# Kernel tuning notes

Hardware: AMD Instinct MI355X
Metric: run time of the kernel (lower is better)

The kernel has to match this reference:

```python
import jax, jax.numpy as jnp
import numpy as np

B, HW, ENC = 64, 14, 2048
T_CAP, VOCAB = 25, 10000
EMB = DEC = ATT = 512


def setup_inputs() -> dict:
    key = jax.random.key(0)
    ks = jax.random.split(key, 24)
    n = lambda k, shape, s=0.02: jax.random.normal(k, shape, jnp.float32) * s
    encoder_out = jax.random.normal(ks[0], (B, HW, HW, ENC), jnp.float32)
    captions = jax.random.randint(ks[1], (B, T_CAP), 0, VOCAB)
    lens = jax.random.randint(ks[2], (B,), 2, T_CAP + 1)
    caption_lengths = jnp.sort(lens)[::-1].at[0].set(T_CAP)  # sorted desc, max=T_CAP
    return {
        'encoder_out': encoder_out,
        'captions': captions,
        'caption_lengths': caption_lengths,
        'emb': jax.random.uniform(ks[3], (VOCAB, EMB), jnp.float32, -0.1, 0.1),
        'We_att': n(ks[4], (ENC, ATT)), 'be_att': jnp.zeros((ATT,), jnp.float32),
        'Wd_att': n(ks[5], (DEC, ATT)), 'bd_att': jnp.zeros((ATT,), jnp.float32),
        'v_att': n(ks[6], (ATT, 1)),    'bv_att': jnp.zeros((1,), jnp.float32),
        'W_ih': n(ks[7], (4 * DEC, EMB + ENC)), 'b_ih': jnp.zeros((4 * DEC,), jnp.float32),
        'W_hh': n(ks[8], (4 * DEC, DEC)),       'b_hh': jnp.zeros((4 * DEC,), jnp.float32),
        'W_init_h': n(ks[9], (ENC, DEC)),  'b_init_h': jnp.zeros((DEC,), jnp.float32),
        'W_init_c': n(ks[10], (ENC, DEC)), 'b_init_c': jnp.zeros((DEC,), jnp.float32),
        'W_fbeta': n(ks[11], (DEC, ENC)),  'b_fbeta': jnp.zeros((ENC,), jnp.float32),
        'W_fc': jax.random.uniform(ks[12], (DEC, VOCAB), jnp.float32, -0.1, 0.1),
        'b_fc': jnp.zeros((VOCAB,), jnp.float32),
    }


def reference(encoder_out, captions, caption_lengths, emb,
              We_att, be_att, Wd_att, bd_att, v_att, bv_att,
              W_ih, b_ih, W_hh, b_hh,
              W_init_h, b_init_h, W_init_c, b_init_c,
              W_fbeta, b_fbeta, W_fc, b_fc):
    Bn = encoder_out.shape[0]
    enc = encoder_out.reshape(Bn, -1, encoder_out.shape[-1])  # [B, P=196, ENC]
    decode_lengths = caption_lengths - 1
    T = captions.shape[1] - 1  # static max(decode_lengths)

    emb_cap = emb[captions]                    # [B, T+1, EMB]
    mean_enc = enc.mean(axis=1)                # [B, ENC]
    h0 = mean_enc @ W_init_h + b_init_h        # [B, DEC]
    c0 = mean_enc @ W_init_c + b_init_c
    att1 = enc @ We_att + be_att               # [B, P, ATT], hoisted (same math each step)

    def step(carry, inp):
        h, c = carry
        x_emb, active = inp                    # [B,EMB], [B] bool (batch_size_t mask)
        # attention
        att2 = h @ Wd_att + bd_att             # [B, ATT]
        e = (jax.nn.relu(att1 + att2[:, None, :]) @ v_att)[..., 0] + bv_att[0]  # [B, P]
        alpha = jax.nn.softmax(e, axis=1)
        ctx = jnp.einsum('bp,bpe->be', alpha, enc)
        # gated context
        ctx = jax.nn.sigmoid(h @ W_fbeta + b_fbeta) * ctx
        # LSTMCell (torch gate order i, f, g, o)
        x = jnp.concatenate([x_emb, ctx], axis=1)
        g = x @ W_ih.T + b_ih + h @ W_hh.T + b_hh
        i_g, f_g, g_g, o_g = jnp.split(g, 4, axis=1)
        c_new = jax.nn.sigmoid(f_g) * c + jax.nn.sigmoid(i_g) * jnp.tanh(g_g)
        h_new = jax.nn.sigmoid(o_g) * jnp.tanh(c_new)
        pred = h_new @ W_fc + b_fc             # dropout = identity (eval)
        m = active[:, None]
        pred = jnp.where(m, pred, 0.0)         # padded rows stay zero (as in torch)
        alpha = jnp.where(m, alpha, 0.0)
        h = jnp.where(m, h_new, h)
        c = jnp.where(m, c_new, c)
        return (h, c), (pred, alpha)

    active_ts = jnp.arange(T)[:, None] < decode_lengths[None, :]   # [T, B]
    xs = (jnp.swapaxes(emb_cap[:, :T], 0, 1), active_ts)
    _, (preds, alphas) = jax.lax.scan(step, (h0, c0), xs)
    predictions = jnp.swapaxes(preds, 0, 1)    # [B, T, VOCAB]
    alphas = jnp.swapaxes(alphas, 0, 1)        # [B, T, P]
    return predictions, captions, decode_lengths, alphas
```

## Files before the change

### kernel.cpp

```cpp
#include <hip/hip_runtime.h>
#include <hip/hip_bf16.h>

#define BATCH 64
#define NPIX 196
#define ENCD 2048
#define ATTD 512
#define DECD 512
#define EMBD 512
#define NVOCAB 10000
#define TSTEPS 24
#define KX 3072
#define NPAD 10112

typedef short bf16x8 __attribute__((ext_vector_type(8)));
typedef float f32x4 __attribute__((ext_vector_type(4)));

__device__ inline ushort f2bf(float f) {
    union { float f; unsigned u; } v; v.f = f;
    unsigned r = (v.u + 0x7fff + ((v.u >> 16) & 1)) >> 16;
    return (ushort)r;
}
__device__ inline float bf2f(ushort u) {
    union { unsigned u; float f; } v; v.u = ((unsigned)u) << 16;
    return v.f;
}

__global__ __launch_bounds__(256) void k_prep(
        const float* __restrict__ Wih, const float* __restrict__ Whh,
        const float* __restrict__ Wd, const float* __restrict__ Wfb,
        const float* __restrict__ Wfc, const float* __restrict__ We,
        const float* __restrict__ emb, const int* __restrict__ caps,
        const int* __restrict__ lens,
        ushort* __restrict__ WTj, ushort* __restrict__ BpreT,
        ushort* __restrict__ WfcT, ushort* __restrict__ WeT,
        ushort* __restrict__ embpartb, float* __restrict__ hcacc,
        float* __restrict__ cap_out, float* __restrict__ len_out) {
    __shared__ float tile[32][33];
    int blk = blockIdx.x, tid = threadIdx.x;
    if (blk < 2048) {
        int j = blk;
        for (int k = tid; k < KX; k += 256) {
            float v = (k < 2560) ? Wih[(size_t)j * 2560 + k] : Whh[(size_t)j * 512 + (k - 2560)];
            WTj[(size_t)j * KX + k] = f2bf(v);
        }
        if (blk == 0) {
            for (int i = tid; i < 1664; i += 256) {
                if (i < 1600) cap_out[i] = (float)caps[i];
                else          len_out[i - 1600] = (float)(lens[i - 1600] - 1);
            }
        }
    } else if (blk < 3328) {
        int i = blk - 2048;
        int nb = (i % 80) * 32, kb = (i / 80) * 32;
        int tx = tid & 31, ty = tid >> 5;
        for (int s = 0; s < 32; s += 8) {
            int k = kb + ty + s, n = nb + tx;
            float v = (n < ATTD) ? Wd[(size_t)k * ATTD + n] : Wfb[(size_t)k * ENCD + (n - ATTD)];
            tile[ty + s][tx] = v;
        }
        __syncthreads();
        for (int s = 0; s < 32; s += 8)
            BpreT[(size_t)(nb + ty + s) * 512 + kb + tx] = f2bf(tile[tx][ty + s]);
    } else if (blk < 8384) {
        int i = blk - 3328;
        int nb = (i % 316) * 32, kb = (i / 316) * 32;
        int tx = tid & 31, ty = tid >> 5;
        for (int s = 0; s < 32; s += 8) {
            int k = kb + ty + s, n = nb + tx;
            float v = (n < NVOCAB) ? Wfc[(size_t)k * NVOCAB + n] : 0.f;
            tile[ty + s][tx] = v;
        }
        __syncthreads();
        for (int s = 0; s < 32; s += 8)
            WfcT[(size_t)(nb + ty + s) * 512 + kb + tx] = f2bf(tile[tx][ty + s]);
    } else if (blk < 9408) {
        int i = blk - 8384;
        int nb = (i % 16) * 32, kb = (i / 16) * 32;
        int tx = tid & 31, ty = tid >> 5;
        for (int s = 0; s < 32; s += 8) {
            int k = kb + ty + s, n = nb + tx;
            tile[ty + s][tx] = We[(size_t)k * ATTD + n];
        }
        __syncthreads();
        for (int s = 0; s < 32; s += 8)
            WeT[(size_t)(nb + ty + s) * ENCD + kb + tx] = f2bf(tile[tx][ty + s]);
    } else if (blk < 10176) {
        int i = blk - 9408;
        int r0 = (i % 24) * 64;
        int n0 = (i / 24) * 64;
        int w = tid >> 6, l = tid & 63;
        int m = l & 15, kg = l >> 4;
        int n = n0 + w * 16 + m;
        const float* Bp = Wih + (size_t)n * 2560 + kg * 8;
        int tok[4];
#pragma unroll
        for (int mf = 0; mf < 4; ++mf) {
            int row = r0 + m + mf * 16;
            tok[mf] = caps[(row & 63) * 25 + (row >> 6)];
        }
        f32x4 acc[4] = {};
        for (int k0 = 0; k0 < 512; k0 += 32) {
            float4 b0 = *(const float4*)(Bp + k0);
            float4 b1 = *(const float4*)(Bp + k0 + 4);
            bf16x8 bb;
            bb[0] = f2bf(b0.x); bb[1] = f2bf(b0.y); bb[2] = f2bf(b0.z); bb[3] = f2bf(b0.w);
            bb[4] = f2bf(b1.x); bb[5] = f2bf(b1.y); bb[6] = f2bf(b1.z); bb[7] = f2bf(b1.w);
#pragma unroll
            for (int mf = 0; mf < 4; ++mf) {
                const float* ap = emb + (size_t)tok[mf] * 512 + kg * 8 + k0;
                float4 f0 = *(const float4*)ap;
                float4 f1 = *(const float4*)(ap + 4);
                bf16x8 a;
                a[0] = f2bf(f0.x); a[1] = f2bf(f0.y); a[2] = f2bf(f0.z); a[3] = f2bf(f0.w);
                a[4] = f2bf(f1.x); a[5] = f2bf(f1.y); a[6] = f2bf(f1.z); a[7] = f2bf(f1.w);
                acc[mf] = __builtin_amdgcn_mfma_f32_16x16x32_bf16(a, bb, acc[mf], 0, 0, 0);
            }
        }
#pragma unroll
        for (int mf = 0; mf < 4; ++mf)
#pragma unroll
            for (int r = 0; r < 4; ++r)
                embpartb[(size_t)(r0 + mf * 16 + kg * 4 + r) * 2048 + n] = f2bf(acc[mf][r]);
    } else {
        int i = blk - 10176;
        for (int j = tid; j < 2048; j += 256) hcacc[(size_t)i * 2048 + j] = 0.f;
    }
}

__global__ void k_encconv(const float* __restrict__ enc, ushort* __restrict__ encb) {
    size_t i = ((size_t)blockIdx.x * 256 + threadIdx.x) * 8;
    float4 f0 = *(const float4*)(enc + i);
    float4 f1 = *(const float4*)(enc + i + 4);
    union { bf16x8 v; ushort u[8]; } o;
    o.u[0] = f2bf(f0.x); o.u[1] = f2bf(f0.y); o.u[2] = f2bf(f0.z); o.u[3] = f2bf(f0.w);
    o.u[4] = f2bf(f1.x); o.u[5] = f2bf(f1.y); o.u[6] = f2bf(f1.z); o.u[7] = f2bf(f1.w);
    *(bf16x8*)(encb + i) = o.v;
}

__global__ __launch_bounds__(256) void k_meanb(const ushort* __restrict__ encb,
                                               ushort* __restrict__ meanb) {
    int b = blockIdx.x, half = blockIdx.y;
    int e0 = half * 1024 + threadIdx.x * 4;
    const ushort* ep = encb + (size_t)b * NPIX * ENCD + e0;
    float s0 = 0.f, s1 = 0.f, s2 = 0.f, s3 = 0.f;
#pragma unroll 4
    for (int p = 0; p < NPIX; ++p) {
        ushort4 v = *(const ushort4*)(ep + (size_t)p * ENCD);
        s0 += bf2f(v.x); s1 += bf2f(v.y); s2 += bf2f(v.z); s3 += bf2f(v.w);
    }
    const float sc = 1.0f / NPIX;
    ushort4 o;
    o.x = f2bf(s0 * sc); o.y = f2bf(s1 * sc); o.z = f2bf(s2 * sc); o.w = f2bf(s3 * sc);
    *(ushort4*)(meanb + (size_t)b * ENCD + e0) = o;
}

__global__ __launch_bounds__(256) void k_initp(
        const ushort* __restrict__ meanb,
        const float* __restrict__ Wh, const float* __restrict__ Wc,
        float* __restrict__ hcacc) {
    __shared__ float mm[4][256];
    int bg = blockIdx.x * 4;
    int jy = blockIdx.y;
    int kz = blockIdx.z;
    int tid = threadIdx.x;
    for (int i = tid; i < 1024; i += 256) {
        int qq = i >> 8, k = i & 255;
        mm[qq][k] = bf2f(meanb[(size_t)(bg + qq) * ENCD + kz * 256 + k]);
    }
    __syncthreads();
    int j = jy * 256 + tid;
    const float* W; int col;
    if (j < 512) { W = Wh; col = j; } else { W = Wc; col = j - 512; }
    W += (size_t)(kz * 256) * 512 + col;
    float acc[4] = {};
    for (int k = 0; k < 256; ++k) {
        float w = W[(size_t)k * 512];
#pragma unroll
        for (int qq = 0; qq < 4; ++qq) acc[qq] += mm[qq][k] * w;
    }
#pragma unroll
    for (int qq = 0; qq < 4; ++qq)
        atomicAdd(hcacc + (size_t)(bg + qq) * 1024 + j, acc[qq]);
}

__global__ __launch_bounds__(256) void k_initfin(
        const float* __restrict__ hcacc, const float* __restrict__ bh,
        const float* __restrict__ bc, ushort* __restrict__ hbf,
        float* __restrict__ c) {
    int base = blockIdx.x * 2048;
    for (int i = threadIdx.x; i < 2048; i += 256) {
        int idx = base + i;
        int b = idx >> 10, n = idx & 1023;
        float v = hcacc[idx];
        if (n < 512) hbf[(size_t)b * 512 + n] = f2bf(v + bh[n]);
        else         c[(size_t)b * 512 + (n - 512)] = v + bc[n - 512];
    }
}

__global__ __launch_bounds__(256) void k_att1(
        const ushort* __restrict__ encb, const ushort* __restrict__ WeT,
        const float* __restrict__ be, ushort* __restrict__ att1b) {
    int w = threadIdx.x >> 6, l = threadIdx.x & 63;
    int wr = w >> 1, wc = w & 1;
    int m0 = blockIdx.x * 128 + wr * 64;
    int n0 = blockIdx.y * 128 + wc * 64;
    int ml = l & 15, kg = l >> 4;
    const ushort* aBase = encb + (size_t)(m0 + ml) * ENCD + kg * 8;
    const ushort* bBase = WeT + (size_t)(n0 + ml) * ENCD + kg * 8;
    f32x4 acc[4][4] = {};
    for (int k0 = 0; k0 < ENCD; k0 += 32) {
        bf16x8 bfr[4], afr[4];
#pragma unroll
        for (int nf = 0; nf < 4; ++nf)
            bfr[nf] = *(const bf16x8*)(bBase + (size_t)nf * 16 * ENCD + k0);
#pragma unroll
        for (int mf = 0; mf < 4; ++mf)
            afr[mf] = *(const bf16x8*)(aBase + (size_t)mf * 16 * ENCD + k0);
#pragma unroll
        for (int mf = 0; mf < 4; ++mf)
#pragma unroll
            for (int nf = 0; nf < 4; ++nf)
                acc[mf][nf] = __builtin_amdgcn_mfma_f32_16x16x32_bf16(afr[mf], bfr[nf], acc[mf][nf], 0, 0, 0);
    }
#pragma unroll
    for (int mf = 0; mf < 4; ++mf)
#pragma unroll
        for (int nf = 0; nf < 4; ++nf) {
            int col = n0 + nf * 16 + ml;
            float bias = be[col];
#pragma unroll
            for (int r = 0; r < 4; ++r) {
                int row = m0 + mf * 16 + kg * 4 + r;
                att1b[(size_t)row * ATTD + col] = f2bf(acc[mf][nf][r] + bias);
            }
        }
}

__global__ __launch_bounds__(512) void k_hsmall2(
        const ushort* __restrict__ hb_cur, const ushort* __restrict__ BpreT,
        const float* __restrict__ bd, const float* __restrict__ bfb,
        float* __restrict__ att2, ushort* __restrict__ gateb) {
    __shared__ float part[2][64][68];
    int blk = blockIdx.x;
    int tid = threadIdx.x;
    int w = tid >> 6, l = tid & 63;
    int wq = w & 3, kh = w >> 2;
    int m = l & 15, kg = l >> 4;
    int n = blk * 64 + wq * 16 + m;
    const ushort* B = BpreT + (size_t)n * 512 + kh * 256 + kg * 8;
    const ushort* A = hb_cur + (size_t)m * 512 + kh * 256 + kg * 8;
    f32x4 acc[4] = {};
#pragma unroll
    for (int k0 = 0; k0 < 256; k0 += 32) {
        bf16x8 bfr = *(const bf16x8*)(B + k0);
#pragma unroll
        for (int mf = 0; mf < 4; ++mf) {
            bf16x8 afr = *(const bf16x8*)(A + mf * 16 * 512 + k0);
            acc[mf] = __builtin_amdgcn_mfma_f32_16x16x32_bf16(afr, bfr, acc[mf], 0, 0, 0);
        }
    }
#pragma unroll
    for (int mf = 0; mf < 4; ++mf)
#pragma unroll
        for (int r = 0; r < 4; ++r)
            part[kh][mf * 16 + kg * 4 + r][wq * 16 + m] = acc[mf][r];
    __syncthreads();
    for (int idx = tid; idx < 4096; idx += 512) {
        int b = idx >> 6, nn = idx & 63;
        float v = part[0][b][nn] + part[1][b][nn];
        int ng = blk * 64 + nn;
        if (ng < 512) att2[(size_t)b * 512 + ng] = v + bd[ng];
        else {
            int e = ng - 512;
            gateb[(size_t)b * 2048 + e] = f2bf(1.f / (1.f + __expf(-(v + bfb[e]))));
        }
    }
}

__global__ __launch_bounds__(512) void k_scorectx(
        const ushort* __restrict__ att1b, const float* __restrict__ att2,
        const float* __restrict__ vatt, const float* __restrict__ bv,
        const ushort* __restrict__ gateb, const int* __restrict__ lens,
        const ushort* __restrict__ encb,
        ushort* __restrict__ ctxb, float* __restrict__ alpha_out, int t) {
    __shared__ float ev[200];
    __shared__ float cpart[4][512];
    __shared__ float inv_s;
    int bid = blockIdx.x;
    int b = bid >> 2, q = bid & 3;
    int tid = threadIdx.x;
    int w = tid >> 6, l = tid & 63;
    {
        float a2r[8], vvr[8];
        const float* att2b = att2 + (size_t)b * ATTD;
#pragma unroll
        for (int i = 0; i < 8; ++i) {
            a2r[i] = att2b[l * 8 + i];
            vvr[i] = vatt[l * 8 + i];
        }
        float bv0 = bv[0];
        for (int pp = w; pp < NPIX; pp += 8) {
            bf16x8 f = *(const bf16x8*)(att1b + ((size_t)b * NPIX + pp) * ATTD + l * 8);
            float s = 0.f;
#pragma unroll
            for (int i = 0; i < 8; ++i)
                s += fmaxf(bf2f((ushort)f[i]) + a2r[i], 0.f) * vvr[i];
            for (int off = 32; off > 0; off >>= 1) s += __shfl_down(s, off);
            if (l == 0) ev[pp] = s + bv0;
        }
    }
    __syncthreads();
    if (w == 0) {
        float mx = -1e30f;
        for (int pp = l; pp < NPIX; pp += 64) mx = fmaxf(mx, ev[pp]);
        for (int off = 32; off > 0; off >>= 1) mx = fmaxf(mx, __shfl_down(mx, off));
        mx = __shfl(mx, 0);
        float s = 0.f;
        for (int pp = l; pp < NPIX; pp += 64) {
            float e_ = __expf(ev[pp] - mx);
            ev[pp] = e_;
            s += e_;
        }
        for (int off = 32; off > 0; off >>= 1) s += __shfl_down(s, off);
        if (l == 0) inv_s = 1.0f / s;
    }
    __syncthreads();
    float inv = inv_s;
    if (q == 0 && tid < NPIX) {
        bool active = t < (lens[b] - 1);
        alpha_out[((size_t)b * TSTEPS + t) * NPIX + tid] = active ? ev[tid] * inv : 0.f;
    }
    {
        int pg = tid >> 7, th = tid & 127;
        const ushort* ep = encb + (size_t)b * NPIX * ENCD + q * 512 + th * 4;
        float s0 = 0.f, s1 = 0.f, s2 = 0.f, s3 = 0.f;
        for (int pp = pg; pp < NPIX; pp += 4) {
            ushort4 v = *(const ushort4*)(ep + (size_t)pp * ENCD);
            float al = ev[pp];
            s0 += al * bf2f(v.x); s1 += al * bf2f(v.y);
            s2 += al * bf2f(v.z); s3 += al * bf2f(v.w);
        }
        cpart[pg][th * 4 + 0] = s0;
        cpart[pg][th * 4 + 1] = s1;
        cpart[pg][th * 4 + 2] = s2;
        cpart[pg][th * 4 + 3] = s3;
    }
    __syncthreads();
    if (tid < 128) {
        ushort4 g4 = *(const ushort4*)(gateb + (size_t)b * 2048 + q * 512 + tid * 4);
        ushort4 o;
        o.x = f2bf((cpart[0][tid * 4 + 0] + cpart[1][tid * 4 + 0] + cpart[2][tid * 4 + 0] + cpart[3][tid * 4 + 0]) * inv * bf2f(g4.x));
        o.y = f2bf((cpart[0][tid * 4 + 1] + cpart[1][tid * 4 + 1] + cpart[2][tid * 4 + 1] + cpart[3][tid * 4 + 1]) * inv * bf2f(g4.y));
        o.z = f2bf((cpart[0][tid * 4 + 2] + cpart[1][tid * 4 + 2] + cpart[2][tid * 4 + 2] + cpart[3][tid * 4 + 2]) * inv * bf2f(g4.z));
        o.w = f2bf((cpart[0][tid * 4 + 3] + cpart[1][tid * 4 + 3] + cpart[2][tid * 4 + 3] + cpart[3][tid * 4 + 3]) * inv * bf2f(g4.w));
        *(ushort4*)(ctxb + (size_t)b * 2048 + q * 512 + tid * 4) = o;
    }
}

__global__ __launch_bounds__(512) void k_gates2(
        const ushort* __restrict__ ctxb, const ushort* __restrict__ hb_cur,
        const ushort* __restrict__ WTj, const ushort* __restrict__ embpartb,
        const float* __restrict__ bih, const float* __restrict__ bhh,
        const int* __restrict__ lens, float* __restrict__ c,
        ushort* __restrict__ hb_nxt, ushort* __restrict__ hAll, int t) {
    __shared__ float part[8][64][16];
    int g = blockIdx.x;
    int tid = threadIdx.x;
    int w = tid >> 6, l = tid & 63;
    int m = l & 15, kg = l >> 4;
    int jrow = (m >> 2) * 512 + g * 4 + (m & 3);
    const ushort* Brow = WTj + (size_t)jrow * KX;
    f32x4 acc[4] = {};
    {
        const ushort* B = Brow + 512 + w * 256 + kg * 8;
        const ushort* A = ctxb + (size_t)m * 2048 + w * 256 + kg * 8;
#pragma unroll
        for (int k0 = 0; k0 < 256; k0 += 32) {
            bf16x8 bfr = *(const bf16x8*)(B + k0);
#pragma unroll
            for (int mf = 0; mf < 4; ++mf) {
                bf16x8 afr = *(const bf16x8*)(A + (size_t)mf * 16 * 2048 + k0);
                acc[mf] = __builtin_amdgcn_mfma_f32_16x16x32_bf16(afr, bfr, acc[mf], 0, 0, 0);
            }
        }
    }
    if (w < 2) {
        const ushort* B = Brow + 2560 + w * 256 + kg * 8;
        const ushort* A = hb_cur + (size_t)m * 512 + w * 256 + kg * 8;
#pragma unroll
        for (int k0 = 0; k0 < 256; k0 += 32) {
            bf16x8 bfr = *(const bf16x8*)(B + k0);
#pragma unroll
            for (int mf = 0; mf < 4; ++mf) {
                bf16x8 afr = *(const bf16x8*)(A + (size_t)mf * 16 * 512 + k0);
                acc[mf] = __builtin_amdgcn_mfma_f32_16x16x32_bf16(afr, bfr, acc[mf], 0, 0, 0);
            }
        }
    }
#pragma unroll
    for (int mf = 0; mf < 4; ++mf)
#pragma unroll
        for (int r = 0; r < 4; ++r)
            part[w][mf * 16 + kg * 4 + r][m] = acc[mf][r];
    __syncthreads();
    if (tid < 256) {
        int bb = tid >> 2, j = tid & 3;
        int d = g * 4 + j;
        float gi = 0.f, gf = 0.f, gg = 0.f, go = 0.f;
#pragma unroll
        for (int w8 = 0; w8 < 8; ++w8) {
            gi += part[w8][bb][j];
            gf += part[w8][bb][4 + j];
            gg += part[w8][bb][8 + j];
            go += part[w8][bb][12 + j];
        }
        ushort hout = hb_cur[(size_t)bb * 512 + d];
        if (t < lens[bb] - 1) {
            const ushort* eb = embpartb + ((size_t)t * 64 + bb) * 2048;
            gi += bf2f(eb[d])        + bih[d]        + bhh[d];
            gf += bf2f(eb[512 + d])  + bih[512 + d]  + bhh[512 + d];
            gg += bf2f(eb[1024 + d]) + bih[1024 + d] + bhh[1024 + d];
            go += bf2f(eb[1536 + d]) + bih[1536 + d] + bhh[1536 + d];
            float cc = c[(size_t)bb * 512 + d];
            float si = 1.f / (1.f + __expf(-gi));
            float sf = 1.f / (1.f + __expf(-gf));
            float so = 1.f / (1.f + __expf(-go));
            float cn = sf * cc + si * tanhf(gg);
            float hn = so * tanhf(cn);
            c[(size_t)bb * 512 + d] = cn;
            hout = f2bf(hn);
        }
        hb_nxt[(size_t)bb * 512 + d] = hout;
        hAll[((size_t)t * 64 + bb) * 512 + d] = hout;
    }
}

__global__ __launch_bounds__(256) void k_predall(
        const ushort* __restrict__ hAll, const ushort* __restrict__ WfcT,
        const float* __restrict__ bfc, const int* __restrict__ lens,
        float* __restrict__ pred) {
    int w = threadIdx.x >> 6, l = threadIdx.x & 63;
    int wr = w >> 1, wc = w & 1;
    int m0 = blockIdx.x * 128 + wr * 64;
    int n0 = blockIdx.y * 128 + wc * 64;
    int ml = l & 15, kg = l >> 4;
    const ushort* aBase = hAll + (size_t)(m0 + ml) * 512 + kg * 8;
    const ushort* bBase = WfcT + (size_t)(n0 + ml) * 512 + kg * 8;
    f32x4 acc[4][4] = {};
#pragma unroll 2
    for (int k0 = 0; k0 < 512; k0 += 32) {
        bf16x8 bfr[4], afr[4];
#pragma unroll
        for (int nf = 0; nf < 4; ++nf)
            bfr[nf] = *(const bf16x8*)(bBase + (size_t)nf * 16 * 512 + k0);
#pragma unroll
        for (int mf = 0; mf < 4; ++mf)
            afr[mf] = *(const bf16x8*)(aBase + (size_t)mf * 16 * 512 + k0);
#pragma unroll
        for (int mf = 0; mf < 4; ++mf)
#pragma unroll
            for (int nf = 0; nf < 4; ++nf)
                acc[mf][nf] = __builtin_amdgcn_mfma_f32_16x16x32_bf16(afr[mf], bfr[nf], acc[mf][nf], 0, 0, 0);
    }
#pragma unroll
    for (int mf = 0; mf < 4; ++mf)
#pragma unroll
        for (int nf = 0; nf < 4; ++nf) {
            int col = n0 + nf * 16 + ml;
            if (col < NVOCAB) {
                float bias = bfc[col];
#pragma unroll
                for (int r = 0; r < 4; ++r) {
                    int row = m0 + mf * 16 + kg * 4 + r;
                    int t = row >> 6, b = row & 63;
                    bool act = t < (lens[b] - 1);
                    pred[((size_t)b * TSTEPS + t) * NVOCAB + col] = act ? acc[mf][nf][r] + bias : 0.f;
                }
            }
        }
}

extern "C" void kernel_launch(void* const* d_in, const int* in_sizes, int n_in,
                              void* d_out, int out_size, void* d_ws, size_t ws_size,
                              hipStream_t stream) {
    const float* enc  = (const float*)d_in[0];
    const int*   caps = (const int*)d_in[1];
    const int*   lens = (const int*)d_in[2];
    const float* emb  = (const float*)d_in[3];
    const float* We   = (const float*)d_in[4];
    const float* be   = (const float*)d_in[5];
    const float* Wd   = (const float*)d_in[6];
    const float* bd   = (const float*)d_in[7];
    const float* vatt = (const float*)d_in[8];
    const float* bv   = (const float*)d_in[9];
    const float* Wih  = (const float*)d_in[10];
    const float* bih  = (const float*)d_in[11];
    const float* Whh  = (const float*)d_in[12];
    const float* bhh  = (const float*)d_in[13];
    const float* Winh = (const float*)d_in[14];
    const float* binh = (const float*)d_in[15];
    const float* Winc = (const float*)d_in[16];
    const float* binc = (const float*)d_in[17];
    const float* Wfb  = (const float*)d_in[18];
    const float* bfb  = (const float*)d_in[19];
    const float* Wfc  = (const float*)d_in[20];
    const float* bfc  = (const float*)d_in[21];

    float* out       = (float*)d_out;
    float* pred_out  = out;
    float* cap_out   = out + 15360000;
    float* len_out   = out + 15361600;
    float* alpha_out = out + 15361664;

    char* p = (char*)d_ws;
    ushort* att1b    = (ushort*)p; p += (size_t)12544 * 512 * 2;
    ushort* WTj      = (ushort*)p; p += (size_t)2048 * KX * 2;
    ushort* WfcT     = (ushort*)p; p += (size_t)NPAD * 512 * 2;
    ushort* BpreT    = (ushort*)p; p += (size_t)2560 * 512 * 2;
    ushort* WeT      = (ushort*)p; p += (size_t)512 * 2048 * 2;
    ushort* embpartb = (ushort*)p; p += (size_t)1536 * 2048 * 2;
    ushort* hAll     = (ushort*)p; p += (size_t)1536 * 512 * 2;
    ushort* ctxb     = (ushort*)p; p += (size_t)64 * 2048 * 2;
    ushort* hb0      = (ushort*)p; p += (size_t)64 * 512 * 2;
    ushort* hb1      = (ushort*)p; p += (size_t)64 * 512 * 2;
    float* c         = (float*)p;  p += (size_t)64 * 512 * 4;
    ushort* meanb    = (ushort*)p; p += (size_t)64 * 2048 * 2;
    float* att2      = (float*)p;  p += (size_t)64 * 512 * 4;
    ushort* gateb    = (ushort*)p; p += (size_t)64 * 2048 * 2;
    ushort* encb     = (ushort*)p; p += (size_t)64 * NPIX * ENCD * 2;
    float* hcacc     = (float*)ctxb;

    k_prep<<<10208, 256, 0, stream>>>(Wih, Whh, Wd, Wfb, Wfc, We, emb, caps, lens,
                                      WTj, BpreT, WfcT, WeT, embpartb, hcacc,
                                      cap_out, len_out);
    k_encconv<<<12544, 256, 0, stream>>>(enc, encb);
    k_meanb<<<dim3(64, 2), 256, 0, stream>>>(encb, meanb);
    k_initp<<<dim3(16, 4, 8), 256, 0, stream>>>(meanb, Winh, Winc, hcacc);
    k_initfin<<<32, 256, 0, stream>>>(hcacc, binh, binc, hb0, c);
    k_att1<<<dim3(98, 4), 256, 0, stream>>>(encb, WeT, be, att1b);

    for (int t = 0; t < TSTEPS; ++t) {
        const ushort* hcur = (t & 1) ? hb1 : hb0;
        ushort* hnxt = (t & 1) ? hb0 : hb1;
        k_hsmall2<<<40, 512, 0, stream>>>(hcur, BpreT, bd, bfb, att2, gateb);
        k_scorectx<<<256, 512, 0, stream>>>(att1b, att2, vatt, bv, gateb, lens,
                                            encb, ctxb, alpha_out, t);
        k_gates2<<<128, 512, 0, stream>>>(ctxb, hcur, WTj, embpartb, bih, bhh,
                                          lens, c, hnxt, hAll, t);
    }
    k_predall<<<dim3(12, 79), 256, 0, stream>>>(hAll, WfcT, bfc, lens, pred_out);
}
```

Measured before the change: 1.903 ms.

## Fuse decoder-state projections into attention-context kernel, drop separate hsmall launch

Merges the per-step hidden-state projection kernel (att2 and the sigmoid gate) into the score/context kernel. Each block recomputes the 64x512 projections with MFMA, keeps only its own batch row in LDS, and no longer round-trips att2 and gate through global memory. This removes one launch and one global sync per step. In exchange every one of the 256 blocks redundantly reads about 1 MB of projection weights and repeats the full small GEMM. Separately, the prep kernel stops converting the first 512 columns of the combined LSTM weight matrix, which are presumably covered by the precomputed embedding part.

```diff
diff --git a/kernel.cpp b/kernel.cpp
--- a/kernel.cpp
+++ b/kernel.cpp
@@ -39,7 +39,7 @@
     int blk = blockIdx.x, tid = threadIdx.x;
     if (blk < 2048) {
         int j = blk;
-        for (int k = tid; k < KX; k += 256) {
+        for (int k = 512 + tid; k < KX; k += 256) {
             float v = (k < 2560) ? Wih[(size_t)j * 2560 + k] : Whh[(size_t)j * 512 + (k - 2560)];
             WTj[(size_t)j * KX + k] = f2bf(v);
         }
@@ -236,53 +236,15 @@
         }
 }
 
-__global__ __launch_bounds__(512) void k_hsmall2(
-        const ushort* __restrict__ hb_cur, const ushort* __restrict__ BpreT,
+__global__ __launch_bounds__(512) void k_attctx2(
+        const ushort* __restrict__ hb_cur, const ushort* __restrict__ att1b,
+        const ushort* __restrict__ encb, const ushort* __restrict__ BpreT,
+        const float* __restrict__ vatt, const float* __restrict__ bv,
         const float* __restrict__ bd, const float* __restrict__ bfb,
-        float* __restrict__ att2, ushort* __restrict__ gateb) {
-    __shared__ float part[2][64][68];
-    int blk = blockIdx.x;
-    int tid = threadIdx.x;
-    int w = tid >> 6, l = tid & 63;
-    int wq = w & 3, kh = w >> 2;
-    int m = l & 15, kg = l >> 4;
-    int n = blk * 64 + wq * 16 + m;
-    const ushort* B = BpreT + (size_t)n * 512 + kh * 256 + kg * 8;
-    const ushort* A = hb_cur + (size_t)m * 512 + kh * 256 + kg * 8;
-    f32x4 acc[4] = {};
-#pragma unroll
-    for (int k0 = 0; k0 < 256; k0 += 32) {
-        bf16x8 bfr = *(const bf16x8*)(B + k0);
-#pragma unroll
-        for (int mf = 0; mf < 4; ++mf) {
-            bf16x8 afr = *(const bf16x8*)(A + mf * 16 * 512 + k0);
-            acc[mf] = __builtin_amdgcn_mfma_f32_16x16x32_bf16(afr, bfr, acc[mf], 0, 0, 0);
-        }
-    }
-#pragma unroll
-    for (int mf = 0; mf < 4; ++mf)
-#pragma unroll
-        for (int r = 0; r < 4; ++r)
-            part[kh][mf * 16 + kg * 4 + r][wq * 16 + m] = acc[mf][r];
-    __syncthreads();
-    for (int idx = tid; idx < 4096; idx += 512) {
-        int b = idx >> 6, nn = idx & 63;
-        float v = part[0][b][nn] + part[1][b][nn];
-        int ng = blk * 64 + nn;
-        if (ng < 512) att2[(size_t)b * 512 + ng] = v + bd[ng];
-        else {
-            int e = ng - 512;
-            gateb[(size_t)b * 2048 + e] = f2bf(1.f / (1.f + __expf(-(v + bfb[e]))));
-        }
-    }
-}
-
-__global__ __launch_bounds__(512) void k_scorectx(
-        const ushort* __restrict__ att1b, const float* __restrict__ att2,
-        const float* __restrict__ vatt, const float* __restrict__ bv,
-        const ushort* __restrict__ gateb, const int* __restrict__ lens,
-        const ushort* __restrict__ encb,
+        const int* __restrict__ lens,
         ushort* __restrict__ ctxb, float* __restrict__ alpha_out, int t) {
+    __shared__ float att2_lds[512];
+    __shared__ float gate_lds[512];
     __shared__ float ev[200];
     __shared__ float cpart[4][512];
     __shared__ float inv_s;
@@ -290,12 +252,71 @@
     int b = bid >> 2, q = bid & 3;
     int tid = threadIdx.x;
     int w = tid >> 6, l = tid & 63;
+    int m = l & 15, kg = l >> 4;
+
+    {
+        int n0w = w * 64;
+        const ushort* A = hb_cur + (size_t)m * 512 + kg * 8;
+        int kgb = (b & 15) >> 2, mfb = b >> 4, rb = b & 3;
+        {
+            f32x4 acc[4][4] = {};
+            const ushort* B = BpreT + (size_t)(n0w + m) * 512 + kg * 8;
+#pragma unroll 4
+            for (int k0 = 0; k0 < 512; k0 += 32) {
+                bf16x8 bfr[4];
+#pragma unroll
+                for (int nf = 0; nf < 4; ++nf)
+                    bfr[nf] = *(const bf16x8*)(B + (size_t)nf * 16 * 512 + k0);
+#pragma unroll
+                for (int mf = 0; mf < 4; ++mf) {
+                    bf16x8 afr = *(const bf16x8*)(A + (size_t)mf * 16 * 512 + k0);
+#pragma unroll
+                    for (int nf = 0; nf < 4; ++nf)
+                        acc[mf][nf] = __builtin_amdgcn_mfma_f32_16x16x32_bf16(afr, bfr[nf], acc[mf][nf], 0, 0, 0);
+                }
+            }
+            if (kg == kgb) {
+#pragma unroll
+                for (int nf = 0; nf < 4; ++nf) {
+                    int n = n0w + nf * 16 + m;
+                    att2_lds[n] = acc[mfb][nf][rb] + bd[n];
+                }
+            }
+        }
+        {
+            f32x4 acc[4][4] = {};
+            const ushort* B = BpreT + (size_t)(512 + q * 512 + n0w + m) * 512 + kg * 8;
+#pragma unroll 4
+            for (int k0 = 0; k0 < 512; k0 += 32) {
+                bf16x8 bfr[4];
+#pragma unroll
+                for (int nf = 0; nf < 4; ++nf)
+                    bfr[nf] = *(const bf16x8*)(B + (size_t)nf * 16 * 512 + k0);
+#pragma unroll
+                for (int mf = 0; mf < 4; ++mf) {
+                    bf16x8 afr = *(const bf16x8*)(A + (size_t)mf * 16 * 512 + k0);
+#pragma unroll
+                    for (int nf = 0; nf < 4; ++nf)
+                        acc[mf][nf] = __builtin_amdgcn_mfma_f32_16x16x32_bf16(afr, bfr[nf], acc[mf][nf], 0, 0, 0);
+                }
+            }
+            if (kg == kgb) {
+#pragma unroll
+                for (int nf = 0; nf < 4; ++nf) {
+                    int n = n0w + nf * 16 + m;
+                    int e = q * 512 + n;
+                    gate_lds[n] = 1.f / (1.f + __expf(-(acc[mfb][nf][rb] + bfb[e])));
+                }
+            }
+        }
+    }
+    __syncthreads();
+
     {
         float a2r[8], vvr[8];
-        const float* att2b = att2 + (size_t)b * ATTD;
 #pragma unroll
         for (int i = 0; i < 8; ++i) {
-            a2r[i] = att2b[l * 8 + i];
+            a2r[i] = att2_lds[l * 8 + i];
             vvr[i] = vatt[l * 8 + i];
         }
         float bv0 = bv[0];
@@ -347,12 +368,13 @@
     }
     __syncthreads();
     if (tid < 128) {
-        ushort4 g4 = *(const ushort4*)(gateb + (size_t)b * 2048 + q * 512 + tid * 4);
         ushort4 o;
-        o.x = f2bf((cpart[0][tid * 4 + 0] + cpart[1][tid * 4 + 0] + cpart[2][tid * 4 + 0] + cpart[3][tid * 4 + 0]) * inv * bf2f(g4.x));
-        o.y = f2bf((cpart[0][tid * 4 + 1] + cpart[1][tid * 4 + 1] + cpart[2][tid * 4 + 1] + cpart[3][tid * 4 + 1]) * inv * bf2f(g4.y));
-        o.z = f2bf((cpart[0][tid * 4 + 2] + cpart[1][tid * 4 + 2] + cpart[2][tid * 4 + 2] + cpart[3][tid * 4 + 2]) * inv * bf2f(g4.z));
-        o.w = f2bf((cpart[0][tid * 4 + 3] + cpart[1][tid * 4 + 3] + cpart[2][tid * 4 + 3] + cpart[3][tid * 4 + 3]) * inv * bf2f(g4.w));
+        float g0 = gate_lds[tid * 4 + 0], g1 = gate_lds[tid * 4 + 1];
+        float g2 = gate_lds[tid * 4 + 2], g3 = gate_lds[tid * 4 + 3];
+        o.x = f2bf((cpart[0][tid * 4 + 0] + cpart[1][tid * 4 + 0] + cpart[2][tid * 4 + 0] + cpart[3][tid * 4 + 0]) * inv * g0);
+        o.y = f2bf((cpart[0][tid * 4 + 1] + cpart[1][tid * 4 + 1] + cpart[2][tid * 4 + 1] + cpart[3][tid * 4 + 1]) * inv * g1);
+        o.z = f2bf((cpart[0][tid * 4 + 2] + cpart[1][tid * 4 + 2] + cpart[2][tid * 4 + 2] + cpart[3][tid * 4 + 2]) * inv * g2);
+        o.w = f2bf((cpart[0][tid * 4 + 3] + cpart[1][tid * 4 + 3] + cpart[2][tid * 4 + 3] + cpart[3][tid * 4 + 3]) * inv * g3);
         *(ushort4*)(ctxb + (size_t)b * 2048 + q * 512 + tid * 4) = o;
     }
 }
@@ -525,8 +547,6 @@
     ushort* hb1      = (ushort*)p; p += (size_t)64 * 512 * 2;
     float* c         = (float*)p;  p += (size_t)64 * 512 * 4;
     ushort* meanb    = (ushort*)p; p += (size_t)64 * 2048 * 2;
-    float* att2      = (float*)p;  p += (size_t)64 * 512 * 4;
-    ushort* gateb    = (ushort*)p; p += (size_t)64 * 2048 * 2;
     ushort* encb     = (ushort*)p; p += (size_t)64 * NPIX * ENCD * 2;
     float* hcacc     = (float*)ctxb;
 
@@ -542,9 +562,8 @@
     for (int t = 0; t < TSTEPS; ++t) {
         const ushort* hcur = (t & 1) ? hb1 : hb0;
         ushort* hnxt = (t & 1) ? hb0 : hb1;
-        k_hsmall2<<<40, 512, 0, stream>>>(hcur, BpreT, bd, bfb, att2, gateb);
-        k_scorectx<<<256, 512, 0, stream>>>(att1b, att2, vatt, bv, gateb, lens,
-                                            encb, ctxb, alpha_out, t);
+        k_attctx2<<<256, 512, 0, stream>>>(hcur, att1b, encb, BpreT, vatt, bv,
+                                           bd, bfb, lens, ctxb, alpha_out, t);
         k_gates2<<<128, 512, 0, stream>>>(ctxb, hcur, WTj, embpartb, bih, bhh,
                                           lens, c, hnxt, hAll, t);
     }
```

After: 3.268 ms. 1.72x slower.
